# Kernel optimization log

Hardware: AMD Instinct MI355X
Metric: run time of the kernel (lower is better)

Reference implementation:

```python
import jax, jax.numpy as jnp
import numpy as np

N = 100000
E = 50000
NNZ = 300000
F_IN = 128
F_OUT = 128


def setup_inputs() -> dict:
    key = jax.random.key(0)
    ks = jax.random.split(key, 10)
    X = jax.random.normal(ks[0], (N, F_IN), dtype=jnp.float32)
    X0 = jax.random.normal(ks[1], (N, F_IN), dtype=jnp.float32)
    vertex = jax.random.randint(ks[2], (NNZ,), 0, N, dtype=jnp.int32)
    edges = jax.random.randint(ks[3], (NNZ,), 0, E, dtype=jnp.int32)
    # params init per reset_parameters: uniform(0.02, 0.05)
    u = lambda k, s: jax.random.uniform(k, s, jnp.float32, 0.02, 0.05)
    w_b = u(ks[4], (2 * F_IN, F_OUT))
    w_a = u(ks[5], (2 * F_IN, F_OUT))
    w_c = u(ks[6], (2 * F_IN, F_OUT))
    b_b = u(ks[7], (1, F_OUT))
    b_a = u(ks[8], (1, F_OUT))
    b_c = u(ks[9], (1, F_OUT))
    return {"X": X, "vertex": vertex, "edges": edges, "X0": X0,
            "n_edges": E, "w_b": w_b, "w_a": w_a, "w_c": w_c,
            "b_b": b_b, "b_a": b_a, "b_c": b_c}


def reference(X, vertex, edges, X0, n_edges, w_b, w_a, w_c, b_b, b_a, b_c):
    n = X.shape[-2]
    # round 1: node -> hyperedge aggregation (scatter-add by edge id)
    Xve = X[vertex]                                        # [nnz, F]
    Xe = jax.ops.segment_sum(Xve, edges, num_segments=n_edges)  # [E, F]
    # round 2: hyperedge -> node, concat with gathered node features
    Xev = jnp.concatenate([X[vertex], Xe[edges]], axis=-1)  # [nnz, 2F]
    Xv = jax.ops.segment_sum(Xev, vertex, num_segments=n)   # [N, 2F]
    # normalization is Identity (InputNorm=False)
    center = Xv @ w_b + b_b                 # [N, F_OUT]
    aXv = jnp.abs(Xv)
    scope_l = aXv @ w_a + b_a
    scope_r = aXv @ w_c + b_c
    HL = center - scope_l
    HR = center + scope_r
    return (center, HL, HR)
```

## Files before the change

### kernel.cpp

```cpp
#include <hip/hip_runtime.h>
#include <cstddef>
#include <cstdint>

#define F 128
#define E_FIXED 50000
#define SCAN_ELEMS 2048

typedef __attribute__((ext_vector_type(8))) short short8;
typedef __attribute__((ext_vector_type(4))) float f32x4;
typedef __attribute__((ext_vector_type(4))) unsigned int uint32x4;
typedef __attribute__((address_space(3))) unsigned int lds_uint;
typedef const __attribute__((address_space(1))) unsigned int glb_uint;

__device__ inline unsigned short f32_to_bf16(float f) {
  union { float f; unsigned int u; } v; v.f = f;
  unsigned int u = v.u;
  unsigned int r = u + 0x7FFFu + ((u >> 16) & 1u);
  return (unsigned short)(r >> 16);
}

__global__ __launch_bounds__(256) void zero_kernel(int* __restrict__ p, int n4) {
  int i = blockIdx.x * 256 + threadIdx.x;
  if (i < n4) reinterpret_cast<int4*>(p)[i] = make_int4(0, 0, 0, 0);
}

__global__ __launch_bounds__(256) void count_kernel(
    const int* __restrict__ vertex, const int* __restrict__ edges,
    int* __restrict__ cnt, int nnz, int E) {
  int i = blockIdx.x * 256 + threadIdx.x;
  if (i >= nnz) return;
  atomicAdd(cnt + edges[i], 1);
  atomicAdd(cnt + E + vertex[i], 1);
}

__global__ __launch_bounds__(256) void scan_partial_kernel(
    const int* __restrict__ cnt, int* __restrict__ off,
    int* __restrict__ bsum, int L) {
  __shared__ int s[256];
  const int t = threadIdx.x;
  const int base = blockIdx.x * SCAN_ELEMS + t * 8;
  int v[8];
  if (base + 8 <= L) {
    int4 a = *reinterpret_cast<const int4*>(cnt + base);
    int4 b = *reinterpret_cast<const int4*>(cnt + base + 4);
    v[0] = a.x; v[1] = a.y; v[2] = a.z; v[3] = a.w;
    v[4] = b.x; v[5] = b.y; v[6] = b.z; v[7] = b.w;
  } else {
    #pragma unroll
    for (int j = 0; j < 8; ++j) v[j] = (base + j < L) ? cnt[base + j] : 0;
  }
  int tsum = 0;
  #pragma unroll
  for (int j = 0; j < 8; ++j) tsum += v[j];
  s[t] = tsum;
  __syncthreads();
  #pragma unroll
  for (int d = 1; d < 256; d <<= 1) {
    int val = (t >= d) ? s[t - d] : 0;
    __syncthreads();
    s[t] += val;
    __syncthreads();
  }
  int run = s[t] - tsum;
  #pragma unroll
  for (int j = 0; j < 8; ++j) {
    int idx = base + j;
    if (idx < L) off[idx] = run;
    run += v[j];
  }
  if (t == 255) bsum[blockIdx.x] = s[255];
}

__global__ __launch_bounds__(128) void scan_bsum_kernel(
    int* __restrict__ bsum, int nb) {
  __shared__ int s[128];
  int t = threadIdx.x;
  int val = (t < nb) ? bsum[t] : 0;
  s[t] = val;
  __syncthreads();
  #pragma unroll
  for (int d = 1; d < 128; d <<= 1) {
    int x = (t >= d) ? s[t - d] : 0;
    __syncthreads();
    s[t] += x;
    __syncthreads();
  }
  if (t < nb) bsum[t] = s[t] - val;
}

__global__ __launch_bounds__(256) void scan_add_kernel(
    int* __restrict__ off, const int* __restrict__ bsum, int L) {
  int b = blockIdx.x;
  if (b == 0) return;
  int add = bsum[b];
  int base = b * SCAN_ELEMS + threadIdx.x * 8;
  if (base + 8 <= L) {
    int4* p0 = reinterpret_cast<int4*>(off + base);
    int4* p1 = reinterpret_cast<int4*>(off + base + 4);
    int4 a = *p0, c = *p1;
    a.x += add; a.y += add; a.z += add; a.w += add;
    c.x += add; c.y += add; c.z += add; c.w += add;
    *p0 = a; *p1 = c;
  } else {
    #pragma unroll
    for (int j = 0; j < 8; ++j)
      if (base + j < L) off[base + j] += add;
  }
}

__global__ __launch_bounds__(256) void fill_kernel(
    const int* __restrict__ vertex, const int* __restrict__ edges,
    const int* __restrict__ off, int* __restrict__ cur,
    int* __restrict__ csr, int nnz, int E) {
  int i = blockIdx.x * 256 + threadIdx.x;
  if (i >= nnz) return;
  int v = vertex[i], e = edges[i];
  int p = atomicAdd(cur + e, 1);
  csr[off[e] + p] = v;
  int q = atomicAdd(cur + E + v, 1);
  csr[off[E + v] + q] = e;
}

__global__ __launch_bounds__(256) void gather_edge_kernel(
    const float* __restrict__ X, const int* __restrict__ off,
    const int* __restrict__ cnt, const int* __restrict__ csr,
    unsigned short* __restrict__ Xe_b, int E) {
  int gid = blockIdx.x * 256 + threadIdx.x;
  int e = gid >> 6;
  int lane = threadIdx.x & 63;
  if (e >= E) return;
  int start = off[e], n = cnt[e];
  float2 acc = make_float2(0.f, 0.f);
  for (int j = 0; j < n; ++j) {
    int v = csr[start + j];
    float2 x = *reinterpret_cast<const float2*>(X + (size_t)v * F + lane * 2);
    acc.x += x.x; acc.y += x.y;
  }
  unsigned int pk = (unsigned int)f32_to_bf16(acc.x) |
                    ((unsigned int)f32_to_bf16(acc.y) << 16);
  *reinterpret_cast<unsigned int*>(Xe_b + (size_t)e * F + lane * 2) = pk;
}

__global__ __launch_bounds__(256) void gather_vertex_kernel(
    const unsigned short* __restrict__ Xe_b, const int* __restrict__ off,
    const int* __restrict__ cnt, const int* __restrict__ csr,
    unsigned short* __restrict__ Xv2_b, int E, int N) {
  int gid = blockIdx.x * 256 + threadIdx.x;
  int v = gid >> 6;
  int lane = threadIdx.x & 63;
  if (v >= N) return;
  int start = off[E + v], n = cnt[E + v];
  float2 acc = make_float2(0.f, 0.f);
  for (int j = 0; j < n; ++j) {
    int e = csr[start + j];
    unsigned int u = *reinterpret_cast<const unsigned int*>(
        Xe_b + (size_t)e * F + lane * 2);
    union { unsigned int u; float f; } lo, hi;
    lo.u = u << 16; hi.u = u & 0xFFFF0000u;
    acc.x += lo.f; acc.y += hi.f;
  }
  unsigned int pk = (unsigned int)f32_to_bf16(acc.x) |
                    ((unsigned int)f32_to_bf16(acc.y) << 16);
  *reinterpret_cast<unsigned int*>(Xv2_b + (size_t)v * F + lane * 2) = pk;
}

__global__ __launch_bounds__(256) void convert_w_kernel(
    const float* __restrict__ wb, const float* __restrict__ wa,
    const float* __restrict__ wc, unsigned short* __restrict__ wt) {
  int id = blockIdx.x * 256 + threadIdx.x;
  int mat = id >> 15;
  int r = id & 32767;
  int k = r >> 7;
  int col = r & 127;
  int ks = k >> 5;
  int kg = (k >> 3) & 3;
  int e  = k & 7;
  int ct = col >> 4;
  int bc = col & 15;
  int lane = kg * 16 + bc;
  const float* w = (mat == 0) ? wb : ((mat == 1) ? wa : wc);
  size_t off = ((((size_t)(ks * 3 + mat) * 8 + ct) * 64 + lane) * 8 + e);
  wt[off] = f32_to_bf16(w[r]);
}

__global__ __launch_bounds__(512, 4) void fused_mfma_kernel(
    const float* __restrict__ X,
    const unsigned short* __restrict__ Xv2_b,
    const int* __restrict__ deg,
    const unsigned short* __restrict__ wt,
    const float* __restrict__ bb, const float* __restrict__ ba,
    const float* __restrict__ bc,
    float* __restrict__ out, int N) {
  __shared__ unsigned short wlds[48 * 512];
  const int t = threadIdx.x;
  const int wave = t >> 6;
  const int lane = t & 63;
  const int node0 = blockIdx.x * 128;
  const int node = node0 + wave * 16 + (lane & 15);
  const int kg = lane >> 4;

  uint32x4 a[8];
  const bool ok = node < N;
  const float dg = ok ? (float)deg[node] : 0.f;
  #pragma unroll
  for (int ks = 0; ks < 4; ++ks) {
    float4 f0 = make_float4(0.f, 0.f, 0.f, 0.f);
    float4 f1 = make_float4(0.f, 0.f, 0.f, 0.f);
    if (ok) {
      const float* src = X + (size_t)node * F + ks * 32 + kg * 8;
      f0 = *reinterpret_cast<const float4*>(src);
      f1 = *reinterpret_cast<const float4*>(src + 4);
      f0.x *= dg; f0.y *= dg; f0.z *= dg; f0.w *= dg;
      f1.x *= dg; f1.y *= dg; f1.z *= dg; f1.w *= dg;
    }
    uint32x4 p;
    p[0] = (unsigned int)f32_to_bf16(f0.x) | ((unsigned int)f32_to_bf16(f0.y) << 16);
    p[1] = (unsigned int)f32_to_bf16(f0.z) | ((unsigned int)f32_to_bf16(f0.w) << 16);
    p[2] = (unsigned int)f32_to_bf16(f1.x) | ((unsigned int)f32_to_bf16(f1.y) << 16);
    p[3] = (unsigned int)f32_to_bf16(f1.z) | ((unsigned int)f32_to_bf16(f1.w) << 16);
    a[ks] = p;
  }
  #pragma unroll
  for (int ks = 4; ks < 8; ++ks) {
    uint32x4 p = (uint32x4)(0u);
    if (ok)
      p = *reinterpret_cast<const uint32x4*>(
          Xv2_b + (size_t)node * F + (ks - 4) * 32 + kg * 8);
    a[ks] = p;
  }

  const int nrow0 = node0 + wave * 16 + (lane >> 4) * 4;

  #pragma unroll
  for (int h = 0; h < 4; ++h) {
    #pragma unroll
    for (int i = 0; i < 3; ++i) {
      int p = wave * 3 + i;
      #pragma unroll
      for (int c = 0; c < 2; ++c) {
        int g = p * 8 + h * 2 + c;
        int q = p * 2 + c;
        __builtin_amdgcn_global_load_lds(
            (glb_uint*)(wt + (size_t)g * 512 + lane * 8),
            (lds_uint*)(&wlds[q * 512]), 16, 0, 0);
      }
    }
    __syncthreads();

    f32x4 acc[3][2];
    #pragma unroll
    for (int m = 0; m < 3; ++m)
      #pragma unroll
      for (int c = 0; c < 2; ++c) acc[m][c] = (f32x4)(0.f);

    #pragma unroll
    for (int ks = 0; ks < 8; ++ks) {
      uint32x4 av = a[ks];
      uint32x4 aav = av & 0x7FFF7FFFu;
      short8 A  = __builtin_bit_cast(short8, av);
      short8 AA = __builtin_bit_cast(short8, aav);
      #pragma unroll
      for (int m = 0; m < 3; ++m) {
        short8 Ause = (m == 0) ? A : AA;
        #pragma unroll
        for (int c = 0; c < 2; ++c) {
          int q = (ks * 3 + m) * 2 + c;
          short8 B = *reinterpret_cast<const short8*>(&wlds[q * 512 + lane * 8]);
          acc[m][c] = __builtin_amdgcn_mfma_f32_16x16x32_bf16(Ause, B, acc[m][c], 0, 0, 0);
        }
      }
    }

    #pragma unroll
    for (int c = 0; c < 2; ++c) {
      int col = h * 32 + c * 16 + (lane & 15);
      float vb = bb[col], va = ba[col], vc = bc[col];
      #pragma unroll
      for (int j = 0; j < 4; ++j) {
        int nd = nrow0 + j;
        if (nd < N) {
          float ce = acc[0][c][j] + vb;
          float sl = acc[1][c][j] + va;
          float sr = acc[2][c][j] + vc;
          out[(size_t)nd * F + col] = ce;
          out[((size_t)N + nd) * F + col] = ce - sl;
          out[((size_t)2 * N + nd) * F + col] = ce + sr;
        }
      }
    }
    __syncthreads();
  }
}

extern "C" void kernel_launch(void* const* d_in, const int* in_sizes, int n_in,
                              void* d_out, int out_size, void* d_ws, size_t ws_size,
                              hipStream_t stream) {
  const float* X      = (const float*)d_in[0];
  const int*   vertex = (const int*)d_in[1];
  const int*   edges  = (const int*)d_in[2];
  const float* wb = (const float*)d_in[5];
  const float* wa = (const float*)d_in[6];
  const float* wc = (const float*)d_in[7];
  const float* bb = (const float*)d_in[8];
  const float* ba = (const float*)d_in[9];
  const float* bc = (const float*)d_in[10];

  const int N   = in_sizes[0] / F;
  const int nnz = in_sizes[1];
  const int E   = E_FIXED;
  const int L   = E + N;
  const int nb  = (L + SCAN_ELEMS - 1) / SCAN_ELEMS;

  unsigned short* Xe_b  = (unsigned short*)d_ws;
  unsigned short* Xv2_b = Xe_b + (size_t)E * F;
  unsigned short* wt    = Xv2_b + (size_t)N * F;
  int* cnt  = (int*)(wt + 3 * 32768);
  int* cur  = cnt + L;
  int* off  = cur + L;
  int* bsum = off + L;
  int* csr  = bsum + 128;

  int n4 = (2 * L) / 4;
  zero_kernel<<<(n4 + 255) / 256, 256, 0, stream>>>(cnt, n4);

  convert_w_kernel<<<384, 256, 0, stream>>>(wb, wa, wc, wt);

  int blocks_nnz = (nnz + 255) / 256;
  count_kernel<<<blocks_nnz, 256, 0, stream>>>(vertex, edges, cnt, nnz, E);

  scan_partial_kernel<<<nb, 256, 0, stream>>>(cnt, off, bsum, L);
  scan_bsum_kernel<<<1, 128, 0, stream>>>(bsum, nb);
  scan_add_kernel<<<nb, 256, 0, stream>>>(off, bsum, L);

  fill_kernel<<<blocks_nnz, 256, 0, stream>>>(vertex, edges, off, cur, csr, nnz, E);

  gather_edge_kernel<<<(E * 64 + 255) / 256, 256, 0, stream>>>(
      X, off, cnt, csr, Xe_b, E);
  gather_vertex_kernel<<<(N * 64 + 255) / 256, 256, 0, stream>>>(
      Xe_b, off, cnt, csr, Xv2_b, E, N);

  int blocks_g = (N + 127) / 128;
  fused_mfma_kernel<<<blocks_g, 512, 0, stream>>>(
      X, Xv2_b, cnt + E, wt, bb, ba, bc, (float*)d_out, N);
}
```

Before: 214.4 us.

## Merge init kernels, use single-pass lookback scan, retile MFMA kernel with prefetch

Combines the zeroing and weight-conversion kernels into one launch. The three-kernel scan becomes a single decoupled-lookback scan that uses flag and prefix state in the workspace, which cuts launches. The MFMA kernel now handles 64 nodes per block, with the 8 waves arranged as 4 row groups by 2 column halves. It prefetches the next weight slice into LDS after each epilogue and raises the launch-bounds occupancy hint. The lookback depends on earlier blocks making progress, and halving the node tile doubles how often weights are staged into LDS per node.

New measurement: 314.4 us. 1.47x slower.

```diff
diff --git a/kernel.cpp b/kernel.cpp
--- a/kernel.cpp
+++ b/kernel.cpp
@@ -19,9 +19,31 @@
   return (unsigned short)(r >> 16);
 }
 
-__global__ __launch_bounds__(256) void zero_kernel(int* __restrict__ p, int n4) {
-  int i = blockIdx.x * 256 + threadIdx.x;
-  if (i < n4) reinterpret_cast<int4*>(p)[i] = make_int4(0, 0, 0, 0);
+__global__ __launch_bounds__(256) void init_kernel(
+    int* __restrict__ zp, int n4, int zb,
+    const float* __restrict__ wb, const float* __restrict__ wa,
+    const float* __restrict__ wc, unsigned short* __restrict__ wt) {
+  int b = blockIdx.x;
+  int t = threadIdx.x;
+  if (b < zb) {
+    int i = b * 256 + t;
+    if (i < n4) reinterpret_cast<int4*>(zp)[i] = make_int4(0, 0, 0, 0);
+    return;
+  }
+  int id = (b - zb) * 256 + t;
+  int mat = id >> 15;
+  int r = id & 32767;
+  int k = r >> 7;
+  int col = r & 127;
+  int ks = k >> 5;
+  int kg = (k >> 3) & 3;
+  int e  = k & 7;
+  int ct = col >> 4;
+  int bc = col & 15;
+  int lane = kg * 16 + bc;
+  const float* w = (mat == 0) ? wb : ((mat == 1) ? wa : wc);
+  size_t off = ((((size_t)(ks * 3 + mat) * 8 + ct) * 64 + lane) * 8 + e);
+  wt[off] = f32_to_bf16(w[r]);
 }
 
 __global__ __launch_bounds__(256) void count_kernel(
@@ -33,18 +55,20 @@
   atomicAdd(cnt + E + vertex[i], 1);
 }
 
-__global__ __launch_bounds__(256) void scan_partial_kernel(
+__global__ __launch_bounds__(256) void scan_lookback_kernel(
     const int* __restrict__ cnt, int* __restrict__ off,
-    int* __restrict__ bsum, int L) {
+    int* __restrict__ state, int L) {
   __shared__ int s[256];
+  __shared__ int sprefix;
+  const int b = blockIdx.x;
   const int t = threadIdx.x;
-  const int base = blockIdx.x * SCAN_ELEMS + t * 8;
+  const int base = b * SCAN_ELEMS + t * 8;
   int v[8];
   if (base + 8 <= L) {
-    int4 a = *reinterpret_cast<const int4*>(cnt + base);
-    int4 b = *reinterpret_cast<const int4*>(cnt + base + 4);
-    v[0] = a.x; v[1] = a.y; v[2] = a.z; v[3] = a.w;
-    v[4] = b.x; v[5] = b.y; v[6] = b.z; v[7] = b.w;
+    int4 a0 = *reinterpret_cast<const int4*>(cnt + base);
+    int4 a1 = *reinterpret_cast<const int4*>(cnt + base + 4);
+    v[0] = a0.x; v[1] = a0.y; v[2] = a0.z; v[3] = a0.w;
+    v[4] = a1.x; v[5] = a1.y; v[6] = a1.z; v[7] = a1.w;
   } else {
     #pragma unroll
     for (int j = 0; j < 8; ++j) v[j] = (base + j < L) ? cnt[base + j] : 0;
@@ -61,50 +85,33 @@
     s[t] += val;
     __syncthreads();
   }
-  int run = s[t] - tsum;
+  if (t == 0) {
+    int bsum = s[255];
+    __hip_atomic_store(&state[128 + b], bsum, __ATOMIC_RELAXED, __HIP_MEMORY_SCOPE_AGENT);
+    __hip_atomic_store(&state[b], 1, __ATOMIC_RELEASE, __HIP_MEMORY_SCOPE_AGENT);
+    int prefix = 0;
+    for (int j = b - 1; j >= 0; --j) {
+      int f;
+      do {
+        f = __hip_atomic_load(&state[j], __ATOMIC_ACQUIRE, __HIP_MEMORY_SCOPE_AGENT);
+      } while (f == 0);
+      if (f == 2) {
+        prefix += __hip_atomic_load(&state[256 + j], __ATOMIC_RELAXED, __HIP_MEMORY_SCOPE_AGENT);
+        break;
+      }
+      prefix += __hip_atomic_load(&state[128 + j], __ATOMIC_RELAXED, __HIP_MEMORY_SCOPE_AGENT);
+    }
+    __hip_atomic_store(&state[256 + b], prefix + bsum, __ATOMIC_RELAXED, __HIP_MEMORY_SCOPE_AGENT);
+    __hip_atomic_store(&state[b], 2, __ATOMIC_RELEASE, __HIP_MEMORY_SCOPE_AGENT);
+    sprefix = prefix;
+  }
+  __syncthreads();
+  int run = sprefix + (s[t] - tsum);
   #pragma unroll
   for (int j = 0; j < 8; ++j) {
     int idx = base + j;
     if (idx < L) off[idx] = run;
     run += v[j];
-  }
-  if (t == 255) bsum[blockIdx.x] = s[255];
-}
-
-__global__ __launch_bounds__(128) void scan_bsum_kernel(
-    int* __restrict__ bsum, int nb) {
-  __shared__ int s[128];
-  int t = threadIdx.x;
-  int val = (t < nb) ? bsum[t] : 0;
-  s[t] = val;
-  __syncthreads();
-  #pragma unroll
-  for (int d = 1; d < 128; d <<= 1) {
-    int x = (t >= d) ? s[t - d] : 0;
-    __syncthreads();
-    s[t] += x;
-    __syncthreads();
-  }
-  if (t < nb) bsum[t] = s[t] - val;
-}
-
-__global__ __launch_bounds__(256) void scan_add_kernel(
-    int* __restrict__ off, const int* __restrict__ bsum, int L) {
-  int b = blockIdx.x;
-  if (b == 0) return;
-  int add = bsum[b];
-  int base = b * SCAN_ELEMS + threadIdx.x * 8;
-  if (base + 8 <= L) {
-    int4* p0 = reinterpret_cast<int4*>(off + base);
-    int4* p1 = reinterpret_cast<int4*>(off + base + 4);
-    int4 a = *p0, c = *p1;
-    a.x += add; a.y += add; a.z += add; a.w += add;
-    c.x += add; c.y += add; c.z += add; c.w += add;
-    *p0 = a; *p1 = c;
-  } else {
-    #pragma unroll
-    for (int j = 0; j < 8; ++j)
-      if (base + j < L) off[base + j] += add;
   }
 }
 
@@ -164,26 +171,7 @@
   *reinterpret_cast<unsigned int*>(Xv2_b + (size_t)v * F + lane * 2) = pk;
 }
 
-__global__ __launch_bounds__(256) void convert_w_kernel(
-    const float* __restrict__ wb, const float* __restrict__ wa,
-    const float* __restrict__ wc, unsigned short* __restrict__ wt) {
-  int id = blockIdx.x * 256 + threadIdx.x;
-  int mat = id >> 15;
-  int r = id & 32767;
-  int k = r >> 7;
-  int col = r & 127;
-  int ks = k >> 5;
-  int kg = (k >> 3) & 3;
-  int e  = k & 7;
-  int ct = col >> 4;
-  int bc = col & 15;
-  int lane = kg * 16 + bc;
-  const float* w = (mat == 0) ? wb : ((mat == 1) ? wa : wc);
-  size_t off = ((((size_t)(ks * 3 + mat) * 8 + ct) * 64 + lane) * 8 + e);
-  wt[off] = f32_to_bf16(w[r]);
-}
-
-__global__ __launch_bounds__(512, 4) void fused_mfma_kernel(
+__global__ __launch_bounds__(512, 6) void fused_mfma_kernel(
     const float* __restrict__ X,
     const unsigned short* __restrict__ Xv2_b,
     const int* __restrict__ deg,
@@ -195,9 +183,24 @@
   const int t = threadIdx.x;
   const int wave = t >> 6;
   const int lane = t & 63;
-  const int node0 = blockIdx.x * 128;
-  const int node = node0 + wave * 16 + (lane & 15);
+  const int wr = wave & 3;
+  const int wc2 = wave >> 2;
+  const int node0 = blockIdx.x * 64;
+  const int node = node0 + wr * 16 + (lane & 15);
   const int kg = lane >> 4;
+
+  #pragma unroll
+  for (int i = 0; i < 3; ++i) {
+    int p = wave * 3 + i;
+    #pragma unroll
+    for (int c = 0; c < 2; ++c) {
+      int g = p * 8 + 0 * 2 + c;
+      int q = p * 2 + c;
+      __builtin_amdgcn_global_load_lds(
+          (glb_uint*)(wt + (size_t)g * 512 + lane * 8),
+          (lds_uint*)(&wlds[q * 512]), 16, 0, 0);
+    }
+  }
 
   uint32x4 a[8];
   const bool ok = node < N;
@@ -229,29 +232,15 @@
     a[ks] = p;
   }
 
-  const int nrow0 = node0 + wave * 16 + (lane >> 4) * 4;
+  const int nrow0 = node0 + wr * 16 + (lane >> 4) * 4;
 
   #pragma unroll
   for (int h = 0; h < 4; ++h) {
+    __syncthreads();
+
+    f32x4 acc[3];
     #pragma unroll
-    for (int i = 0; i < 3; ++i) {
-      int p = wave * 3 + i;
-      #pragma unroll
-      for (int c = 0; c < 2; ++c) {
-        int g = p * 8 + h * 2 + c;
-        int q = p * 2 + c;
-        __builtin_amdgcn_global_load_lds(
-            (glb_uint*)(wt + (size_t)g * 512 + lane * 8),
-            (lds_uint*)(&wlds[q * 512]), 16, 0, 0);
-      }
-    }
-    __syncthreads();
-
-    f32x4 acc[3][2];
-    #pragma unroll
-    for (int m = 0; m < 3; ++m)
-      #pragma unroll
-      for (int c = 0; c < 2; ++c) acc[m][c] = (f32x4)(0.f);
+    for (int m = 0; m < 3; ++m) acc[m] = (f32x4)(0.f);
 
     #pragma unroll
     for (int ks = 0; ks < 8; ++ks) {
@@ -262,26 +251,22 @@
       #pragma unroll
       for (int m = 0; m < 3; ++m) {
         short8 Ause = (m == 0) ? A : AA;
-        #pragma unroll
-        for (int c = 0; c < 2; ++c) {
-          int q = (ks * 3 + m) * 2 + c;
-          short8 B = *reinterpret_cast<const short8*>(&wlds[q * 512 + lane * 8]);
-          acc[m][c] = __builtin_amdgcn_mfma_f32_16x16x32_bf16(Ause, B, acc[m][c], 0, 0, 0);
-        }
+        int q = (ks * 3 + m) * 2 + wc2;
+        short8 B = *reinterpret_cast<const short8*>(&wlds[q * 512 + lane * 8]);
+        acc[m] = __builtin_amdgcn_mfma_f32_16x16x32_bf16(Ause, B, acc[m], 0, 0, 0);
       }
     }
 
-    #pragma unroll
-    for (int c = 0; c < 2; ++c) {
-      int col = h * 32 + c * 16 + (lane & 15);
+    {
+      int col = h * 32 + wc2 * 16 + (lane & 15);
       float vb = bb[col], va = ba[col], vc = bc[col];
       #pragma unroll
       for (int j = 0; j < 4; ++j) {
         int nd = nrow0 + j;
         if (nd < N) {
-          float ce = acc[0][c][j] + vb;
-          float sl = acc[1][c][j] + va;
-          float sr = acc[2][c][j] + vc;
+          float ce = acc[0][j] + vb;
+          float sl = acc[1][j] + va;
+          float sr = acc[2][j] + vc;
           out[(size_t)nd * F + col] = ce;
           out[((size_t)N + nd) * F + col] = ce - sl;
           out[((size_t)2 * N + nd) * F + col] = ce + sr;
@@ -289,6 +274,20 @@
       }
     }
     __syncthreads();
+    if (h < 3) {
+      #pragma unroll
+      for (int i = 0; i < 3; ++i) {
+        int p = wave * 3 + i;
+        #pragma unroll
+        for (int c = 0; c < 2; ++c) {
+          int g = p * 8 + (h + 1) * 2 + c;
+          int q = p * 2 + c;
+          __builtin_amdgcn_global_load_lds(
+              (glb_uint*)(wt + (size_t)g * 512 + lane * 8),
+              (lds_uint*)(&wlds[q * 512]), 16, 0, 0);
+        }
+      }
+    }
   }
 }
 
@@ -314,23 +313,20 @@
   unsigned short* Xe_b  = (unsigned short*)d_ws;
   unsigned short* Xv2_b = Xe_b + (size_t)E * F;
   unsigned short* wt    = Xv2_b + (size_t)N * F;
-  int* cnt  = (int*)(wt + 3 * 32768);
-  int* cur  = cnt + L;
-  int* off  = cur + L;
-  int* bsum = off + L;
-  int* csr  = bsum + 128;
-
-  int n4 = (2 * L) / 4;
-  zero_kernel<<<(n4 + 255) / 256, 256, 0, stream>>>(cnt, n4);
-
-  convert_w_kernel<<<384, 256, 0, stream>>>(wb, wa, wc, wt);
+  int* cnt   = (int*)(wt + 3 * 32768);
+  int* cur   = cnt + L;
+  int* state = cur + L;
+  int* off   = state + 384;
+  int* csr   = off + L;
+
+  int n4 = (2 * L + 384) / 4;
+  int zb = (n4 + 255) / 256;
+  init_kernel<<<zb + 384, 256, 0, stream>>>(cnt, n4, zb, wb, wa, wc, wt);
 
   int blocks_nnz = (nnz + 255) / 256;
   count_kernel<<<blocks_nnz, 256, 0, stream>>>(vertex, edges, cnt, nnz, E);
 
-  scan_partial_kernel<<<nb, 256, 0, stream>>>(cnt, off, bsum, L);
-  scan_bsum_kernel<<<1, 128, 0, stream>>>(bsum, nb);
-  scan_add_kernel<<<nb, 256, 0, stream>>>(off, bsum, L);
+  scan_lookback_kernel<<<nb, 256, 0, stream>>>(cnt, off, state, L);
 
   fill_kernel<<<blocks_nnz, 256, 0, stream>>>(vertex, edges, off, cur, csr, nnz, E);
 
@@ -339,7 +335,7 @@
   gather_vertex_kernel<<<(N * 64 + 255) / 256, 256, 0, stream>>>(
       Xe_b, off, cnt, csr, Xv2_b, E, N);
 
-  int blocks_g = (N + 127) / 128;
+  int blocks_g = (N + 63) / 64;
   fused_mfma_kernel<<<blocks_g, 512, 0, stream>>>(
       X, Xv2_b, cnt + E, wt, bb, ba, bc, (float*)d_out, N);
 }
```
